# Kernel optimization log

Hardware: AMD Instinct MI355X
Metric: run time of the kernel (lower is better)

## Reference

```python
import jax, jax.numpy as jnp
import numpy as np

H, DH = 16, 64  # heads, dim_head; inner = H*DH = 1024
EPS = 1e-5


def _ln(t, g, b):
    mu = jnp.mean(t, axis=-1, keepdims=True)
    var = jnp.var(t, axis=-1, keepdims=True)
    return (t - mu) * jax.lax.rsqrt(var + EPS) * g + b


def _split_heads(t):
    b, n, _ = t.shape
    return t.reshape(b, n, H, DH).transpose(0, 2, 1, 3)  # (b,h,n,dh)


def setup_inputs() -> dict:
    key = jax.random.key(0)
    ks = jax.random.split(key, 5)
    B, S, M, D = 16, 64, 4096, 1024  # S must equal DH (see source einsum quirk)
    return {
        "x": jax.random.normal(ks[0], (B, S, D), jnp.float32),
        "latents": jax.random.normal(ks[1], (B, M, D), jnp.float32),
        "ln_x_g": jnp.ones((D,), jnp.float32),
        "ln_x_b": jnp.zeros((D,), jnp.float32),
        "ln_l_g": jnp.ones((D,), jnp.float32),
        "ln_l_b": jnp.zeros((D,), jnp.float32),
        "Wq": jax.random.normal(ks[2], (D, H * DH), jnp.float32) * 0.02,
        "Wkv": jax.random.normal(ks[3], (D, 2 * H * DH), jnp.float32) * 0.02,
        "Wout": jax.random.normal(ks[4], (H * DH, D), jnp.float32) * 0.02,
    }


def reference(x, latents, ln_x_g, ln_x_b, ln_l_g, ln_l_b, Wq, Wkv, Wout):
    scale = DH ** -0.5
    xn = _ln(x, ln_x_g, ln_x_b)          # (B,S,D)
    ln = _ln(latents, ln_l_g, ln_l_b)    # (B,M,D)
    q = _split_heads(ln @ Wq) * scale    # (B,H,M,DH)
    k, v = map(_split_heads, jnp.split(xn @ Wkv, 2, axis=-1))  # (B,H,S,DH)
    sim = jnp.einsum('bhid,bhjd->bhij', q, k)                  # (B,H,M,S)
    sim = sim - jax.lax.stop_gradient(jnp.max(sim, axis=-1, keepdims=True))
    attn = jax.nn.softmax(sim, axis=-1)
    # Faithful to source: einsum('b h i d, b h j d -> b h i j', attn, v)
    # contracts attn's S dim with v's DH dim (requires S == DH); out = attn @ v^T.
    out = jnp.einsum('bhis,bhjs->bhij', attn, v)               # (B,H,M,S)
    b, _, m, _ = out.shape
    out = out.transpose(0, 2, 1, 3).reshape(b, m, H * DH)      # (B,M,inner)
    return out @ Wout                                          # (B,M,D)
```

## Files before the change

### kernel.cpp

```cpp
#include <hip/hip_runtime.h>
#include <stdint.h>

#define B_ 16
#define S_ 64
#define M_ 4096
#define D_ 1024
#define H_ 16
#define DH_ 64

typedef unsigned short ushort_t;
typedef __attribute__((ext_vector_type(8))) __bf16 bfrag;
typedef __attribute__((ext_vector_type(4))) float f32x4;

__device__ __forceinline__ ushort_t f2bf(float f) {
  union { float f; uint32_t u; } v; v.f = f;
  uint32_t r = v.u + 0x7fffu + ((v.u >> 16) & 1u);
  return (ushort_t)(r >> 16);
}

__device__ __forceinline__ void gload_lds16(const void* g, void* l) {
  __builtin_amdgcn_global_load_lds((const __attribute__((address_space(1))) void*)g,
                                   (__attribute__((address_space(3))) void*)l, 16, 0, 0);
}

__device__ __forceinline__ f32x4 mfma16x16x32(bfrag a, bfrag b, f32x4 c) {
  return __builtin_amdgcn_mfma_f32_16x16x32_bf16(a, b, c, 0, 0, 0);
}

__device__ __forceinline__ int fsw(int r) { return (((r >> 2) & 3) << 1) | (r & 1); }

__global__ __launch_bounds__(256) void ln_rows_kernel(
    const float* __restrict__ x, const float* __restrict__ g,
    const float* __restrict__ bta, ushort_t* __restrict__ out) {
  const int row = blockIdx.x;
  const int t = threadIdx.x;
  const float4* xr = (const float4*)(x + (size_t)row * D_);
  float4 v = xr[t];
  float s = v.x + v.y + v.z + v.w;
  float ss = v.x * v.x + v.y * v.y + v.z * v.z + v.w * v.w;
#pragma unroll
  for (int o = 32; o >= 1; o >>= 1) { s += __shfl_down(s, o); ss += __shfl_down(ss, o); }
  __shared__ float red[16];
  const int wid = t >> 6;
  if ((t & 63) == 0) { red[wid] = s; red[8 + wid] = ss; }
  __syncthreads();
  float tot = red[0] + red[1] + red[2] + red[3];
  float tot2 = red[8] + red[9] + red[10] + red[11];
  float mu = tot * (1.0f / D_);
  float var = tot2 * (1.0f / D_) - mu * mu;
  float rstd = rsqrtf(var + 1e-5f);
  float4 gg = ((const float4*)g)[t];
  float4 bb = ((const float4*)bta)[t];
  ushort_t ob[4];
  ob[0] = f2bf((v.x - mu) * rstd * gg.x + bb.x);
  ob[1] = f2bf((v.y - mu) * rstd * gg.y + bb.y);
  ob[2] = f2bf((v.z - mu) * rstd * gg.z + bb.z);
  ob[3] = f2bf((v.w - mu) * rstd * gg.w + bb.w);
  *(uint2*)(out + (size_t)row * D_ + t * 4) = *(const uint2*)ob;
}

__global__ void transpose_cast_kernel(const float* __restrict__ W, ushort_t* __restrict__ WT,
                                      int N, float scale) {
  __shared__ float tile[32][33];
  const int n0 = blockIdx.x * 32, k0 = blockIdx.y * 32;
  const int tx = threadIdx.x, ty = threadIdx.y;
#pragma unroll
  for (int i = ty; i < 32; i += 8)
    tile[i][tx] = W[(size_t)(k0 + i) * N + n0 + tx];
  __syncthreads();
#pragma unroll
  for (int i = ty; i < 32; i += 8)
    WT[(size_t)(n0 + i) * D_ + k0 + tx] = f2bf(tile[tx][i] * scale);
}

__global__ __launch_bounds__(256) void gemm_kv_kernel(
    const ushort_t* __restrict__ A, const ushort_t* __restrict__ Bt,
    ushort_t* __restrict__ kb, ushort_t* __restrict__ vb) {
  __shared__ __align__(16) ushort_t sA[128 * 32];
  __shared__ __align__(16) ushort_t sB[128 * 32];
  const int tid = threadIdx.x, wid = tid >> 6, lane = tid & 63;
  const size_t arow0 = (size_t)blockIdx.x * 128;
  const size_t brow0 = (size_t)blockIdx.y * 128;
  const int wr = (wid >> 1) * 64, wc = (wid & 1) * 64;
  const int srow = tid >> 2, scol = (tid & 3) * 8;
  const ushort_t* ga = A + (arow0 + srow) * (size_t)D_ + scol;
  const ushort_t* gb = Bt + (brow0 + srow) * (size_t)D_ + scol;
  const int frow = lane & 15, kslot = (lane >> 4) * 8;
  f32x4 acc[4][4] = {};
  for (int k0 = 0; k0 < D_; k0 += 32) {
    gload_lds16(ga, sA + wid * 512);
    gload_lds16(ga + 64 * (size_t)D_, sA + 2048 + wid * 512);
    gload_lds16(gb, sB + wid * 512);
    gload_lds16(gb + 64 * (size_t)D_, sB + 2048 + wid * 512);
    ga += 32; gb += 32;
    __syncthreads();
    bfrag af[4], bfv[4];
#pragma unroll
    for (int m = 0; m < 4; ++m)
      af[m] = *(const bfrag*)&sA[(wr + m * 16 + frow) * 32 + kslot];
#pragma unroll
    for (int n = 0; n < 4; ++n)
      bfv[n] = *(const bfrag*)&sB[(wc + n * 16 + frow) * 32 + kslot];
#pragma unroll
    for (int m = 0; m < 4; ++m)
#pragma unroll
      for (int n = 0; n < 4; ++n)
        acc[m][n] = mfma16x16x32(af[m], bfv[n], acc[m][n]);
    __syncthreads();
  }
  const int erow = (lane >> 4) * 4, ecol = lane & 15;
#pragma unroll
  for (int m = 0; m < 4; ++m)
#pragma unroll
    for (int n = 0; n < 4; ++n)
#pragma unroll
      for (int r = 0; r < 4; ++r) {
        size_t i = arow0 + wr + m * 16 + erow + r;
        int bb = (int)(i >> 6), s = (int)(i & 63);
        size_t n2 = brow0 + wc + n * 16 + ecol;
        ushort_t val = f2bf(acc[m][n][r]);
        ushort_t* dst = (n2 < 1024) ? kb : vb;
        size_t hh = (n2 & 1023) >> 6, d = n2 & 63;
        dst[(((size_t)bb * H_ + hh) * S_ + s) * DH_ + d] = val;
      }
}

template <int MODE>
__global__ __launch_bounds__(512, 2) void gemm256_kernel(
    const ushort_t* __restrict__ A, const ushort_t* __restrict__ Bt,
    const ushort_t* __restrict__ kbuf, const ushort_t* __restrict__ vbuf,
    void* __restrict__ Cout) {
  __shared__ __align__(16) ushort_t lds[65536];
  const int tid = threadIdx.x, wid = tid >> 6, lane = tid & 63;
  const int frow = lane & 15, klo = lane >> 4;
  const int wm = wid >> 2, wn = wid & 3;

  const int l = ((int)blockIdx.x & 7) * 128 + ((int)blockIdx.x >> 3);
  const int mblk = l >> 2, nblk = l & 3;
  const size_t arow0 = (size_t)mblk * 256;
  const size_t bcol0 = (size_t)nblk * 256;

  const int srow = tid >> 3;
  const int sgsw = tid & 7;
  const int G = sgsw ^ (srow & 7);
  const int side = G >> 2, g2 = G & 3;
  const ushort_t* pA = A + (arow0 + (size_t)(side * 128 + srow)) * D_ + g2 * 8;
  const ushort_t* pB = Bt + (bcol0 + (size_t)((side * 2 + (srow >> 5)) * 64 + (srow & 31))) * D_ + g2 * 8;

#define STAGE(KT)                                                                  \
  do {                                                                             \
    const int _s = (KT) & 3;                                                       \
    const size_t _kn = (size_t)(((KT) < 32 ? (KT) : 31)) * 32;                     \
    gload_lds16(pB + _kn, &lds[32768 + _s * 8192 + wid * 512]);                    \
    gload_lds16(pB + 32 * (size_t)D_ + _kn, &lds[32768 + _s * 8192 + 4096 + wid * 512]); \
    gload_lds16(pA + _kn, &lds[_s * 8192 + wid * 512]);                            \
    gload_lds16(pA + 64 * (size_t)D_ + _kn, &lds[_s * 8192 + 4096 + wid * 512]);   \
  } while (0)

  STAGE(0);
  STAGE(1);
  STAGE(2);

  f32x4 acc[8][4] = {};
  for (int kt = 0; kt < 32; ++kt) {
    asm volatile("s_waitcnt vmcnt(8)" ::: "memory");
    __builtin_amdgcn_s_barrier();
    __builtin_amdgcn_sched_barrier(0);
    STAGE(kt + 3);
    const int sl = kt & 3;
    bfrag ar[8], br[4];
#pragma unroll
    for (int mf = 0; mf < 8; ++mf) {
      const int i = (mf & 3) * 16 + frow;
      const int gsw = (wm * 4 + klo) ^ (i & 7);
      ar[mf] = *(const bfrag*)&lds[sl * 8192 + (mf >> 2) * 4096 + i * 64 + gsw * 8];
    }
#pragma unroll
    for (int nf = 0; nf < 4; ++nf) {
      const int t = (wn & 1) * 32 + (nf & 1) * 16 + frow;
      const int gsw = ((wn >> 1) * 4 + klo) ^ (t & 7);
      br[nf] = *(const bfrag*)&lds[32768 + sl * 8192 + (nf >> 1) * 4096 + t * 64 + gsw * 8];
    }
    __builtin_amdgcn_s_setprio(1);
#pragma unroll
    for (int mf = 0; mf < 8; ++mf)
#pragma unroll
      for (int nf = 0; nf < 4; ++nf)
        acc[mf][nf] = mfma16x16x32(ar[mf], br[nf], acc[mf][nf]);
    __builtin_amdgcn_s_setprio(0);
  }
  asm volatile("s_waitcnt vmcnt(0)" ::: "memory");
  __builtin_amdgcn_s_barrier();
  __builtin_amdgcn_sched_barrier(0);
#undef STAGE

  if constexpr (MODE == 0) {
    float* C = (float*)Cout;
#pragma unroll
    for (int m = 0; m < 8; ++m)
#pragma unroll
      for (int n = 0; n < 4; ++n)
#pragma unroll
        for (int r = 0; r < 4; ++r)
          C[(arow0 + wm * 128 + m * 16 + klo * 4 + r) * 1024 + bcol0 + wn * 64 + n * 16 + frow] =
              acc[m][n][r];
  } else {
    ushort_t* W = &lds[wid * 4096];
    ushort_t* out1 = (ushort_t*)Cout;
    const int head = nblk * 4 + wn;
    const int bbatch = mblk >> 4;
    const size_t kvbase = ((size_t)bbatch * H_ + head) * (size_t)(S_ * DH_);
    bfrag kb[4][2], vb[4][2];
#pragma unroll
    for (int nf = 0; nf < 4; ++nf)
#pragma unroll
      for (int kk = 0; kk < 2; ++kk) {
        kb[nf][kk] = *(const bfrag*)&kbuf[kvbase + (nf * 16 + frow) * 64 + kk * 32 + klo * 8];
        vb[nf][kk] = *(const bfrag*)&vbuf[kvbase + (nf * 16 + frow) * 64 + kk * 32 + klo * 8];
      }
#pragma unroll
    for (int hh = 0; hh < 2; ++hh) {
#pragma unroll
      for (int m2 = 0; m2 < 4; ++m2)
#pragma unroll
        for (int r = 0; r < 4; ++r) {
          const int row = m2 * 16 + klo * 4 + r;
          const int fs = fsw(row);
#pragma unroll
          for (int n = 0; n < 4; ++n) {
            const int cc = n * 16 + frow;
            W[row * 64 + ((((cc >> 3) ^ fs) << 3) | (cc & 7))] = f2bf(acc[hh * 4 + m2][n][r]);
          }
        }
      f32x4 s[4][4] = {};
#pragma unroll
      for (int m2 = 0; m2 < 4; ++m2) {
        const int row = m2 * 16 + frow;
        const int fs = fsw(row);
#pragma unroll
        for (int kk = 0; kk < 2; ++kk) {
          bfrag qa = *(const bfrag*)&W[row * 64 + (((kk * 4 + klo) ^ fs) << 3)];
#pragma unroll
          for (int nf = 0; nf < 4; ++nf)
            s[m2][nf] = mfma16x16x32(qa, kb[nf][kk], s[m2][nf]);
        }
      }
#pragma unroll
      for (int m2 = 0; m2 < 4; ++m2)
#pragma unroll
        for (int r = 0; r < 4; ++r) {
          float a0 = s[m2][0][r], a1 = s[m2][1][r], a2 = s[m2][2][r], a3 = s[m2][3][r];
          float mx = fmaxf(fmaxf(a0, a1), fmaxf(a2, a3));
#pragma unroll
          for (int o = 1; o < 16; o <<= 1) mx = fmaxf(mx, __shfl_xor(mx, o));
          a0 = __expf(a0 - mx); a1 = __expf(a1 - mx);
          a2 = __expf(a2 - mx); a3 = __expf(a3 - mx);
          float sm = (a0 + a1) + (a2 + a3);
#pragma unroll
          for (int o = 1; o < 16; o <<= 1) sm += __shfl_xor(sm, o);
          const float inv = 1.0f / sm;
          s[m2][0][r] = a0 * inv; s[m2][1][r] = a1 * inv;
          s[m2][2][r] = a2 * inv; s[m2][3][r] = a3 * inv;
        }
#pragma unroll
      for (int m2 = 0; m2 < 4; ++m2)
#pragma unroll
        for (int r = 0; r < 4; ++r) {
          const int row = m2 * 16 + klo * 4 + r;
          const int fs = fsw(row);
#pragma unroll
          for (int n = 0; n < 4; ++n) {
            const int cc = n * 16 + frow;
            W[row * 64 + ((((cc >> 3) ^ fs) << 3) | (cc & 7))] = f2bf(s[m2][n][r]);
          }
        }
      f32x4 o[4][4] = {};
#pragma unroll
      for (int m2 = 0; m2 < 4; ++m2) {
        const int row = m2 * 16 + frow;
        const int fs = fsw(row);
#pragma unroll
        for (int kk = 0; kk < 2; ++kk) {
          bfrag pa = *(const bfrag*)&W[row * 64 + (((kk * 4 + klo) ^ fs) << 3)];
#pragma unroll
          for (int nf = 0; nf < 4; ++nf)
            o[m2][nf] = mfma16x16x32(pa, vb[nf][kk], o[m2][nf]);
        }
      }
#pragma unroll
      for (int m2 = 0; m2 < 4; ++m2)
#pragma unroll
        for (int r = 0; r < 4; ++r) {
          const int row = m2 * 16 + klo * 4 + r;
          const int fs = fsw(row);
#pragma unroll
          for (int n = 0; n < 4; ++n) {
            const int cc = n * 16 + frow;
            W[row * 64 + ((((cc >> 3) ^ fs) << 3) | (cc & 7))] = f2bf(o[m2][n][r]);
          }
        }
      const size_t grow0 = arow0 + wm * 128 + hh * 64;
#pragma unroll
      for (int it = 0; it < 8; ++it) {
        const int idx = it * 64 + lane;
        const int rr = idx >> 3, gs = idx & 7;
        const int gcol = (gs ^ fsw(rr)) << 3;
        *(uint4*)&out1[(grow0 + rr) * 1024 + head * 64 + gcol] =
            *(const uint4*)&W[rr * 64 + gs * 8];
      }
    }
  }
}

extern "C" void kernel_launch(void* const* d_in, const int* in_sizes, int n_in,
                              void* d_out, int out_size, void* d_ws, size_t ws_size,
                              hipStream_t stream) {
  const float* x = (const float*)d_in[0];
  const float* lat = (const float*)d_in[1];
  const float* lxg = (const float*)d_in[2];
  const float* lxb = (const float*)d_in[3];
  const float* llg = (const float*)d_in[4];
  const float* llb = (const float*)d_in[5];
  const float* Wq = (const float*)d_in[6];
  const float* Wkv = (const float*)d_in[7];
  const float* Wout = (const float*)d_in[8];
  float* out = (float*)d_out;
  char* ws = (char*)d_ws;

  ushort_t* xn = (ushort_t*)(ws);
  ushort_t* wqT = (ushort_t*)(ws + (2ull << 20));
  ushort_t* wkvT = (ushort_t*)(ws + (4ull << 20));
  ushort_t* woT = (ushort_t*)(ws + (8ull << 20));
  ushort_t* kbuf = (ushort_t*)(ws + (10ull << 20));
  ushort_t* vbuf = (ushort_t*)(ws + (12ull << 20));
  ushort_t* out1 = (ushort_t*)(ws + (14ull << 20));
  ushort_t* lnl = (ushort_t*)d_out;

  dim3 tb(32, 8);
  transpose_cast_kernel<<<dim3(1024 / 32, 32), tb, 0, stream>>>(Wq, wqT, 1024, 0.125f);
  transpose_cast_kernel<<<dim3(2048 / 32, 32), tb, 0, stream>>>(Wkv, wkvT, 2048, 1.0f);
  transpose_cast_kernel<<<dim3(1024 / 32, 32), tb, 0, stream>>>(Wout, woT, 1024, 1.0f);
  ln_rows_kernel<<<B_ * S_, 256, 0, stream>>>(x, lxg, lxb, xn);
  ln_rows_kernel<<<B_ * M_, 256, 0, stream>>>(lat, llg, llb, lnl);
  gemm_kv_kernel<<<dim3(8, 16), 256, 0, stream>>>(xn, wkvT, kbuf, vbuf);
  gemm256_kernel<1><<<1024, 512, 0, stream>>>(lnl, wqT, kbuf, vbuf, out1);
  gemm256_kernel<0><<<1024, 512, 0, stream>>>(out1, woT, nullptr, nullptr, out);
}
```

Before: 477.1 us.

## Split GEMM mainloop into half-tile phases interleaving loads, LDS reads and MFMA

Restructures the 256x256 GEMM mainloop into four phases per two k-steps. Each phase issues half of the next stage's global-to-LDS loads, reads half of the A fragments, and runs a 4x4 MFMA block with barriers around it. The LDS layout also changes to 32-element rows with a new XOR swizzle, and B fragments are reused across the two M-halves. The aim is to overlap memory traffic and LDS reads with MFMA work more finely, at the cost of extra barriers per iteration.

```diff
diff --git a/kernel.cpp b/kernel.cpp
--- a/kernel.cpp
+++ b/kernel.cpp
@@ -140,59 +140,74 @@
   const size_t arow0 = (size_t)mblk * 256;
   const size_t bcol0 = (size_t)nblk * 256;
 
-  const int srow = tid >> 3;
-  const int sgsw = tid & 7;
-  const int G = sgsw ^ (srow & 7);
-  const int side = G >> 2, g2 = G & 3;
-  const ushort_t* pA = A + (arow0 + (size_t)(side * 128 + srow)) * D_ + g2 * 8;
-  const ushort_t* pB = Bt + (bcol0 + (size_t)((side * 2 + (srow >> 5)) * 64 + (srow & 31))) * D_ + g2 * 8;
-
-#define STAGE(KT)                                                                  \
-  do {                                                                             \
-    const int _s = (KT) & 3;                                                       \
-    const size_t _kn = (size_t)(((KT) < 32 ? (KT) : 31)) * 32;                     \
-    gload_lds16(pB + _kn, &lds[32768 + _s * 8192 + wid * 512]);                    \
-    gload_lds16(pB + 32 * (size_t)D_ + _kn, &lds[32768 + _s * 8192 + 4096 + wid * 512]); \
-    gload_lds16(pA + _kn, &lds[_s * 8192 + wid * 512]);                            \
-    gload_lds16(pA + 64 * (size_t)D_ + _kn, &lds[_s * 8192 + 4096 + wid * 512]);   \
+  const int r0 = tid >> 2;
+  const int gsrc = (tid & 3) ^ ((tid >> 3) & 3);
+  const ushort_t* pA0 = A + (arow0 + r0) * (size_t)D_ + gsrc * 8;
+  const ushort_t* pA1 = pA0 + (size_t)128 * D_;
+  const ushort_t* pB0 = Bt + (bcol0 + r0) * (size_t)D_ + gsrc * 8;
+  const ushort_t* pB1 = pB0 + (size_t)128 * D_;
+  const int rasw = (klo ^ ((frow >> 1) & 3)) * 8;
+
+#define STAGE_A(G)                                                            \
+  do {                                                                        \
+    const int s_ = (G) & 3;                                                   \
+    const size_t ko_ = (size_t)((G) < 32 ? (G) : 31) * 32;                    \
+    gload_lds16(pA0 + ko_, &lds[s_ * 8192 + wid * 512]);                      \
+    gload_lds16(pA1 + ko_, &lds[s_ * 8192 + 4096 + wid * 512]);               \
   } while (0)
-
-  STAGE(0);
-  STAGE(1);
-  STAGE(2);
+#define STAGE_B(G)                                                            \
+  do {                                                                        \
+    const int s_ = (G) & 3;                                                   \
+    const size_t ko_ = (size_t)((G) < 32 ? (G) : 31) * 32;                    \
+    gload_lds16(pB0 + ko_, &lds[32768 + s_ * 8192 + wid * 512]);              \
+    gload_lds16(pB1 + ko_, &lds[32768 + s_ * 8192 + 4096 + wid * 512]);       \
+  } while (0)
+
+#define PHASE(KH, MH, STAGE_STMT, DO_WAIT)                                    \
+  do {                                                                        \
+    STAGE_STMT;                                                               \
+    const ushort_t* As_ = &lds[((2 * t + (KH)) & 3) * 8192];                  \
+    if ((MH) == 0) {                                                          \
+      const ushort_t* Bs_ = &lds[32768 + ((2 * t + (KH)) & 3) * 8192];        \
+      _Pragma("unroll") for (int nf = 0; nf < 4; ++nf)                        \
+          bregs[nf] = *(const bfrag*)&Bs_[(wn * 64 + nf * 16 + frow) * 32 + rasw]; \
+    }                                                                         \
+    bfrag a_[4];                                                              \
+    _Pragma("unroll") for (int mf = 0; mf < 4; ++mf)                          \
+        a_[mf] = *(const bfrag*)&As_[(wm * 128 + (MH) * 64 + mf * 16 + frow) * 32 + rasw]; \
+    if (DO_WAIT) asm volatile("s_waitcnt vmcnt(8)" ::: "memory");             \
+    __builtin_amdgcn_s_barrier();                                             \
+    asm volatile("s_waitcnt lgkmcnt(0)" ::: "memory");                        \
+    __builtin_amdgcn_sched_barrier(0);                                        \
+    __builtin_amdgcn_s_setprio(1);                                            \
+    _Pragma("unroll") for (int mf = 0; mf < 4; ++mf)                          \
+        _Pragma("unroll") for (int nf = 0; nf < 4; ++nf)                      \
+            acc[(MH) * 4 + mf][nf] =                                          \
+                mfma16x16x32(a_[mf], bregs[nf], acc[(MH) * 4 + mf][nf]);      \
+    __builtin_amdgcn_s_setprio(0);                                            \
+    __builtin_amdgcn_s_barrier();                                             \
+  } while (0)
+
+  STAGE_A(0); STAGE_B(0);
+  STAGE_A(1); STAGE_B(1);
+  STAGE_A(2); STAGE_B(2);
+  asm volatile("s_waitcnt vmcnt(8)" ::: "memory");
+  __builtin_amdgcn_s_barrier();
 
   f32x4 acc[8][4] = {};
-  for (int kt = 0; kt < 32; ++kt) {
-    asm volatile("s_waitcnt vmcnt(8)" ::: "memory");
-    __builtin_amdgcn_s_barrier();
-    __builtin_amdgcn_sched_barrier(0);
-    STAGE(kt + 3);
-    const int sl = kt & 3;
-    bfrag ar[8], br[4];
-#pragma unroll
-    for (int mf = 0; mf < 8; ++mf) {
-      const int i = (mf & 3) * 16 + frow;
-      const int gsw = (wm * 4 + klo) ^ (i & 7);
-      ar[mf] = *(const bfrag*)&lds[sl * 8192 + (mf >> 2) * 4096 + i * 64 + gsw * 8];
-    }
-#pragma unroll
-    for (int nf = 0; nf < 4; ++nf) {
-      const int t = (wn & 1) * 32 + (nf & 1) * 16 + frow;
-      const int gsw = ((wn >> 1) * 4 + klo) ^ (t & 7);
-      br[nf] = *(const bfrag*)&lds[32768 + sl * 8192 + (nf >> 1) * 4096 + t * 64 + gsw * 8];
-    }
-    __builtin_amdgcn_s_setprio(1);
-#pragma unroll
-    for (int mf = 0; mf < 8; ++mf)
-#pragma unroll
-      for (int nf = 0; nf < 4; ++nf)
-        acc[mf][nf] = mfma16x16x32(ar[mf], br[nf], acc[mf][nf]);
-    __builtin_amdgcn_s_setprio(0);
+  bfrag bregs[4];
+  for (int t = 0; t < 16; ++t) {
+    PHASE(0, 0, STAGE_A(2 * t + 3), 0);
+    PHASE(0, 1, STAGE_B(2 * t + 3), 1);
+    PHASE(1, 0, STAGE_A(2 * t + 4), 0);
+    PHASE(1, 1, STAGE_B(2 * t + 4), 1);
   }
   asm volatile("s_waitcnt vmcnt(0)" ::: "memory");
   __builtin_amdgcn_s_barrier();
   __builtin_amdgcn_sched_barrier(0);
-#undef STAGE
+#undef PHASE
+#undef STAGE_A
+#undef STAGE_B
 
   if constexpr (MODE == 0) {
     float* C = (float*)Cout;
```

New measurement: 472.7 us. No clear change (-0.9%).

## Shrink GEMM tile to 256x128 with four waves and double-buffered LDS

Applied to the files above, without the earlier changes.

Replaces the 256x256, 512-thread GEMM block and its 4-stage LDS ring with a 256x128, 256-thread block and a 2-stage double buffer. It also switches to a new XOR swizzle and adds a second barrier per k-step before issuing the next prefetch. The smaller LDS footprint (48KB instead of 128KB) lets more blocks stay resident per CU, which is meant to improve latency hiding and load balance across 2048 blocks. In exchange, each A tile is reloaded twice as often and the pipeline depth is shallower.

```diff
diff --git a/kernel.cpp b/kernel.cpp
--- a/kernel.cpp
+++ b/kernel.cpp
@@ -126,72 +126,70 @@
 }
 
 template <int MODE>
-__global__ __launch_bounds__(512, 2) void gemm256_kernel(
+__global__ __launch_bounds__(256, 2) void gemm128_kernel(
     const ushort_t* __restrict__ A, const ushort_t* __restrict__ Bt,
     const ushort_t* __restrict__ kbuf, const ushort_t* __restrict__ vbuf,
     void* __restrict__ Cout) {
-  __shared__ __align__(16) ushort_t lds[65536];
+  __shared__ __align__(16) ushort_t lds[24576];
   const int tid = threadIdx.x, wid = tid >> 6, lane = tid & 63;
   const int frow = lane & 15, klo = lane >> 4;
-  const int wm = wid >> 2, wn = wid & 3;
-
-  const int l = ((int)blockIdx.x & 7) * 128 + ((int)blockIdx.x >> 3);
-  const int mblk = l >> 2, nblk = l & 3;
+  const int wm = wid >> 1, wn = wid & 1;
+
+  const int l = ((int)blockIdx.x & 7) * 256 + ((int)blockIdx.x >> 3);
+  const int mblk = l >> 3, nblk = l & 7;
   const size_t arow0 = (size_t)mblk * 256;
-  const size_t bcol0 = (size_t)nblk * 256;
-
-  const int srow = tid >> 3;
-  const int sgsw = tid & 7;
-  const int G = sgsw ^ (srow & 7);
-  const int side = G >> 2, g2 = G & 3;
-  const ushort_t* pA = A + (arow0 + (size_t)(side * 128 + srow)) * D_ + g2 * 8;
-  const ushort_t* pB = Bt + (bcol0 + (size_t)((side * 2 + (srow >> 5)) * 64 + (srow & 31))) * D_ + g2 * 8;
-
-#define STAGE(KT)                                                                  \
+  const size_t bcol0 = (size_t)nblk * 128;
+
+  const int r0 = tid >> 2;
+  const int gsrc = (tid & 3) ^ ((tid >> 3) & 3);
+  const ushort_t* pA = A + (arow0 + r0) * (size_t)D_ + gsrc * 8;
+  const ushort_t* pB = Bt + (bcol0 + r0) * (size_t)D_ + gsrc * 8;
+  const int rasw = (klo ^ ((frow >> 1) & 3)) * 8;
+
+#define STAGE(G)                                                                   \
   do {                                                                             \
-    const int _s = (KT) & 3;                                                       \
-    const size_t _kn = (size_t)(((KT) < 32 ? (KT) : 31)) * 32;                     \
-    gload_lds16(pB + _kn, &lds[32768 + _s * 8192 + wid * 512]);                    \
-    gload_lds16(pB + 32 * (size_t)D_ + _kn, &lds[32768 + _s * 8192 + 4096 + wid * 512]); \
-    gload_lds16(pA + _kn, &lds[_s * 8192 + wid * 512]);                            \
-    gload_lds16(pA + 64 * (size_t)D_ + _kn, &lds[_s * 8192 + 4096 + wid * 512]);   \
+    const int s_ = (G) & 1;                                                        \
+    const size_t ko_ = (size_t)((G) < 32 ? (G) : 31) * 32;                         \
+    gload_lds16(pA + ko_, &lds[s_ * 8192 + wid * 512]);                            \
+    gload_lds16(pA + 64 * (size_t)D_ + ko_, &lds[s_ * 8192 + 2048 + wid * 512]);   \
+    gload_lds16(pA + 128 * (size_t)D_ + ko_, &lds[s_ * 8192 + 4096 + wid * 512]);  \
+    gload_lds16(pA + 192 * (size_t)D_ + ko_, &lds[s_ * 8192 + 6144 + wid * 512]);  \
+    gload_lds16(pB + ko_, &lds[16384 + s_ * 4096 + wid * 512]);                    \
+    gload_lds16(pB + 64 * (size_t)D_ + ko_, &lds[16384 + s_ * 4096 + 2048 + wid * 512]); \
   } while (0)
 
   STAGE(0);
   STAGE(1);
-  STAGE(2);
 
   f32x4 acc[8][4] = {};
-  for (int kt = 0; kt < 32; ++kt) {
-    asm volatile("s_waitcnt vmcnt(8)" ::: "memory");
+  for (int g = 0; g < 32; ++g) {
+    asm volatile("s_waitcnt vmcnt(6)" ::: "memory");
     __builtin_amdgcn_s_barrier();
-    __builtin_amdgcn_sched_barrier(0);
-    STAGE(kt + 3);
-    const int sl = kt & 3;
-    bfrag ar[8], br[4];
-#pragma unroll
-    for (int mf = 0; mf < 8; ++mf) {
-      const int i = (mf & 3) * 16 + frow;
-      const int gsw = (wm * 4 + klo) ^ (i & 7);
-      ar[mf] = *(const bfrag*)&lds[sl * 8192 + (mf >> 2) * 4096 + i * 64 + gsw * 8];
-    }
-#pragma unroll
-    for (int nf = 0; nf < 4; ++nf) {
-      const int t = (wn & 1) * 32 + (nf & 1) * 16 + frow;
-      const int gsw = ((wn >> 1) * 4 + klo) ^ (t & 7);
-      br[nf] = *(const bfrag*)&lds[32768 + sl * 8192 + (nf >> 1) * 4096 + t * 64 + gsw * 8];
-    }
+    asm volatile("" ::: "memory");
+    const ushort_t* As = &lds[(g & 1) * 8192];
+    const ushort_t* Bs = &lds[16384 + (g & 1) * 4096];
+    bfrag a_[8], b_[4];
+#pragma unroll
+    for (int mf = 0; mf < 8; ++mf)
+      a_[mf] = *(const bfrag*)&As[(wm * 128 + mf * 16 + frow) * 32 + rasw];
+#pragma unroll
+    for (int nf = 0; nf < 4; ++nf)
+      b_[nf] = *(const bfrag*)&Bs[(wn * 64 + nf * 16 + frow) * 32 + rasw];
     __builtin_amdgcn_s_setprio(1);
 #pragma unroll
     for (int mf = 0; mf < 8; ++mf)
 #pragma unroll
       for (int nf = 0; nf < 4; ++nf)
-        acc[mf][nf] = mfma16x16x32(ar[mf], br[nf], acc[mf][nf]);
+        acc[mf][nf] = mfma16x16x32(a_[mf], b_[nf], acc[mf][nf]);
     __builtin_amdgcn_s_setprio(0);
+    asm volatile("" ::: "memory");
+    __builtin_amdgcn_s_barrier();
+    asm volatile("" ::: "memory");
+    STAGE(g + 2);
   }
   asm volatile("s_waitcnt vmcnt(0)" ::: "memory");
   __builtin_amdgcn_s_barrier();
-  __builtin_amdgcn_sched_barrier(0);
+  asm volatile("" ::: "memory");
 #undef STAGE
 
   if constexpr (MODE == 0) {
@@ -207,7 +205,7 @@
   } else {
     ushort_t* W = &lds[wid * 4096];
     ushort_t* out1 = (ushort_t*)Cout;
-    const int head = nblk * 4 + wn;
+    const int head = nblk * 2 + wn;
     const int bbatch = mblk >> 4;
     const size_t kvbase = ((size_t)bbatch * H_ + head) * (size_t)(S_ * DH_);
     bfrag kb[4][2], vb[4][2];
@@ -343,6 +341,6 @@
   ln_rows_kernel<<<B_ * S_, 256, 0, stream>>>(x, lxg, lxb, xn);
   ln_rows_kernel<<<B_ * M_, 256, 0, stream>>>(lat, llg, llb, lnl);
   gemm_kv_kernel<<<dim3(8, 16), 256, 0, stream>>>(xn, wkvT, kbuf, vbuf);
-  gemm256_kernel<1><<<1024, 512, 0, stream>>>(lnl, wqT, kbuf, vbuf, out1);
-  gemm256_kernel<0><<<1024, 512, 0, stream>>>(out1, woT, nullptr, nullptr, out);
-}
+  gemm128_kernel<1><<<2048, 256, 0, stream>>>(lnl, wqT, kbuf, vbuf, out1);
+  gemm128_kernel<0><<<2048, 256, 0, stream>>>(out1, woT, nullptr, nullptr, out);
+}
```

Measured after the change: 501.3 us. 5.1% more time.
